# Optimization experiments

Measured on AMD Instinct MI355X. Metric: run time of the kernel, lower is better.

The kernel has to match this reference:

```python
import jax, jax.numpy as jnp
import numpy as np

DIM = 512
RANK = 64


def setup_inputs() -> dict:
    key = jax.random.key(0)
    ks = jax.random.split(key, 8)
    B, T, S = 2, 1024, 1024
    target_val = jax.random.normal(ks[0], (B, T, DIM), dtype=jnp.float32)
    source_val = jax.random.normal(ks[1], (B, S, DIM), dtype=jnp.float32)
    # Linear weights stored torch-style [out, in]
    Wt = jax.random.normal(ks[2], (RANK, DIM), dtype=jnp.float32) / np.sqrt(DIM)
    Ws = jax.random.normal(ks[3], (RANK, DIM), dtype=jnp.float32) / np.sqrt(DIM)
    wt_out = jax.random.normal(ks[4], (RANK,), dtype=jnp.float32) / np.sqrt(RANK)
    ws_out = jax.random.normal(ks[5], (RANK,), dtype=jnp.float32) / np.sqrt(RANK)
    interaction_weight = 0.02 * jax.random.normal(ks[6], (RANK,), dtype=jnp.float32)
    bias = jnp.zeros((), dtype=jnp.float32)
    return {
        'target_val': target_val,
        'source_val': source_val,
        'Wt': Wt,
        'Ws': Ws,
        'wt_out': wt_out,
        'ws_out': ws_out,
        'interaction_weight': interaction_weight,
        'bias': bias,
    }


def reference(target_val, source_val, Wt, Ws, wt_out, ws_out, interaction_weight, bias):
    # Project to low-rank width r
    pt = jnp.einsum('btd,rd->btr', target_val, Wt)   # [B,T,R]
    ps = jnp.einsum('bsd,rd->bsr', source_val, Ws)   # [B,S,R]
    target_linear = jnp.einsum('btr,r->bt', pt, wt_out)  # [B,T]
    source_linear = jnp.einsum('bsr,r->bs', ps, ws_out)  # [B,S]
    # Pairwise multiplicative interaction -> SiLU -> rank reduction
    interaction = jax.nn.silu(pt[:, :, None, :] * ps[:, None, :, :])  # [B,T,S,R]
    scores = jnp.einsum('btsr,r->bts', interaction, interaction_weight)
    scores = scores + target_linear[:, :, None] + source_linear[:, None, :] + bias
    return scores
```

## Files before the change

### kernel.cpp

```cpp
#include <hip/hip_runtime.h>

#define DIM   512
#define RANK  64
#define TDIM  1024
#define BB    2
#define NROWS (BB * TDIM)

__device__ __forceinline__ float fast_exp2(float x) { return __builtin_amdgcn_exp2f(x); }
__device__ __forceinline__ float fast_rcp(float x)  { return __builtin_amdgcn_rcpf(x); }

__global__ __launch_bounds__(256)
void proj_kernel(const float* __restrict__ tv, const float* __restrict__ sv,
                 const float* __restrict__ Wt, const float* __restrict__ Ws,
                 float* __restrict__ pt, float* __restrict__ ps)
{
    const int which = blockIdx.z;
    const float* X = which ? sv : tv;
    const float* W = which ? Ws : Wt;
    float* P       = which ? ps : pt;

    const int row0 = blockIdx.x * 64;
    const int kc   = blockIdx.y * 64;
    const int tid  = threadIdx.x;
    const int tx   = tid & 15;
    const int ty   = tid >> 4;

    __shared__ float xs[64][68];
    __shared__ float wsm[64][68];

#pragma unroll
    for (int p = 0; p < 4; p++) {
        const int r = (tid >> 4) + p * 16;
        const int c = (tid & 15) * 4;
        *(float4*)&xs[r][c]  = *(const float4*)&X[(size_t)(row0 + r) * DIM + kc + c];
        *(float4*)&wsm[r][c] = *(const float4*)&W[(size_t)r * DIM + kc + c];
    }
    __syncthreads();

    float acc[4][4];
#pragma unroll
    for (int i = 0; i < 4; i++)
#pragma unroll
        for (int j = 0; j < 4; j++) acc[i][j] = 0.f;

#pragma unroll 2
    for (int k4 = 0; k4 < 64; k4 += 4) {
        float4 a[4], b[4];
#pragma unroll
        for (int i = 0; i < 4; i++) a[i] = *(const float4*)&xs[ty + 16 * i][k4];
#pragma unroll
        for (int j = 0; j < 4; j++) b[j] = *(const float4*)&wsm[tx + 16 * j][k4];
#pragma unroll
        for (int i = 0; i < 4; i++)
#pragma unroll
            for (int j = 0; j < 4; j++) {
                acc[i][j] = fmaf(a[i].x, b[j].x, acc[i][j]);
                acc[i][j] = fmaf(a[i].y, b[j].y, acc[i][j]);
                acc[i][j] = fmaf(a[i].z, b[j].z, acc[i][j]);
                acc[i][j] = fmaf(a[i].w, b[j].w, acc[i][j]);
            }
    }

#pragma unroll
    for (int i = 0; i < 4; i++)
#pragma unroll
        for (int j = 0; j < 4; j++)
            atomicAdd(&P[(size_t)(row0 + ty + 16 * i) * RANK + tx + 16 * j], acc[i][j]);
}

__global__ __launch_bounds__(256)
void pair_kernel(const float* __restrict__ pt, const float* __restrict__ ps,
                 const float* __restrict__ wt_out, const float* __restrict__ ws_out,
                 const float* __restrict__ iw, const float* __restrict__ bias_p,
                 float* __restrict__ out)
{
    const int b  = blockIdx.z;
    const int t0 = blockIdx.y * 64;
    const int s0 = blockIdx.x * 64;
    const int tid = threadIdx.x;
    const int tx  = tid & 15;
    const int ty  = tid >> 4;

    __shared__ float pts[64][68];
    __shared__ float sts[64][68];
    __shared__ __align__(16) float wsh[64];
    __shared__ float tlsh[64];
    __shared__ float slsh[64];

    const float* ptb = pt + ((size_t)b * TDIM + t0) * RANK;
    const float* psb = ps + ((size_t)b * TDIM + s0) * RANK;

#pragma unroll
    for (int p = 0; p < 4; p++) {
        const int r = (tid >> 4) + p * 16;
        const int c = (tid & 15) * 4;
        *(float4*)&pts[r][c] = *(const float4*)&ptb[(size_t)r * RANK + c];
        *(float4*)&sts[r][c] = *(const float4*)&psb[(size_t)r * RANK + c];
    }
    if (tid < 64) wsh[tid] = iw[tid];
    __syncthreads();

    if (tid < 64) {
        float v = 0.f;
#pragma unroll 8
        for (int r = 0; r < RANK; r++) v = fmaf(pts[tid][r], wt_out[r], v);
        tlsh[tid] = v;
    } else if (tid < 128) {
        const int s = tid - 64;
        float v = 0.f;
#pragma unroll 8
        for (int r = 0; r < RANK; r++) v = fmaf(sts[s][r], ws_out[r], v);
        slsh[s] = v;
    }
    __syncthreads();

    const float bias = bias_p[0];

    float acc[4][4];
#pragma unroll
    for (int i = 0; i < 4; i++)
#pragma unroll
        for (int j = 0; j < 4; j++) acc[i][j] = 0.f;

    const float NL2E = -1.44269504088896340736f;

#pragma unroll 2
    for (int r4 = 0; r4 < RANK; r4 += 4) {
        const float4 w4 = *(const float4*)&wsh[r4];
        const float wv[4] = {w4.x, w4.y, w4.z, w4.w};

        float a2[4][4], wa[4][4], bv[4][4];
#pragma unroll
        for (int i = 0; i < 4; i++) {
            const float4 a = *(const float4*)&pts[ty + 16 * i][r4];
            const float av[4] = {a.x, a.y, a.z, a.w};
#pragma unroll
            for (int k = 0; k < 4; k++) {
                a2[i][k] = av[k] * NL2E;
                wa[i][k] = av[k] * wv[k];
            }
        }
#pragma unroll
        for (int j = 0; j < 4; j++) {
            const float4 v = *(const float4*)&sts[tx + 16 * j][r4];
            bv[j][0] = v.x; bv[j][1] = v.y; bv[j][2] = v.z; bv[j][3] = v.w;
        }

#pragma unroll
        for (int i = 0; i < 4; i++)
#pragma unroll
            for (int j = 0; j < 4; j++)
#pragma unroll
                for (int k = 0; k < 4; k++) {
                    const float t  = a2[i][k] * bv[j][k];
                    const float e  = fast_exp2(t);
                    const float rc = fast_rcp(1.0f + e);
                    acc[i][j] = fmaf(wa[i][k] * bv[j][k], rc, acc[i][j]);
                }
    }

#pragma unroll
    for (int i = 0; i < 4; i++) {
        const int t = t0 + ty + 16 * i;
        const float tl = tlsh[ty + 16 * i];
        float* orow = out + ((size_t)b * TDIM + t) * TDIM + s0;
#pragma unroll
        for (int j = 0; j < 4; j++) {
            orow[tx + 16 * j] = acc[i][j] + tl + slsh[tx + 16 * j] + bias;
        }
    }
}

extern "C" void kernel_launch(void* const* d_in, const int* in_sizes, int n_in,
                              void* d_out, int out_size, void* d_ws, size_t ws_size,
                              hipStream_t stream)
{
    const float* tv     = (const float*)d_in[0];
    const float* sv     = (const float*)d_in[1];
    const float* Wt     = (const float*)d_in[2];
    const float* Ws     = (const float*)d_in[3];
    const float* wt_out = (const float*)d_in[4];
    const float* ws_out = (const float*)d_in[5];
    const float* iw     = (const float*)d_in[6];
    const float* bias   = (const float*)d_in[7];
    float* out = (float*)d_out;

    float* pt = (float*)d_ws;
    float* ps = pt + (size_t)NROWS * RANK;

    hipMemsetAsync(d_ws, 0, 2 * (size_t)NROWS * RANK * sizeof(float), stream);

    dim3 pgrid(NROWS / 64, DIM / 64, 2);
    proj_kernel<<<pgrid, 256, 0, stream>>>(tv, sv, Wt, Ws, pt, ps);

    dim3 ggrid(TDIM / 64, TDIM / 64, BB);
    pair_kernel<<<ggrid, 256, 0, stream>>>(pt, ps, wt_out, ws_out, iw, bias, out);
}
```

Measured before the change: 117.9 us.

## Remove split-K atomics in projection and use packed float2 math in pair kernel

```diff
diff --git a/kernel.cpp b/kernel.cpp
--- a/kernel.cpp
+++ b/kernel.cpp
@@ -5,6 +5,9 @@
 #define TDIM  1024
 #define BB    2
 #define NROWS (BB * TDIM)
+
+typedef float v2f __attribute__((ext_vector_type(2)));
+typedef float v4f __attribute__((ext_vector_type(4)));
 
 __device__ __forceinline__ float fast_exp2(float x) { return __builtin_amdgcn_exp2f(x); }
 __device__ __forceinline__ float fast_rcp(float x)  { return __builtin_amdgcn_rcpf(x); }
@@ -14,58 +17,53 @@
                  const float* __restrict__ Wt, const float* __restrict__ Ws,
                  float* __restrict__ pt, float* __restrict__ ps)
 {
-    const int which = blockIdx.z;
+    const int which = blockIdx.y;
     const float* X = which ? sv : tv;
     const float* W = which ? Ws : Wt;
     float* P       = which ? ps : pt;
 
-    const int row0 = blockIdx.x * 64;
-    const int kc   = blockIdx.y * 64;
+    const int row0 = blockIdx.x * 16;
     const int tid  = threadIdx.x;
     const int tx   = tid & 15;
     const int ty   = tid >> 4;
 
-    __shared__ float xs[64][68];
+    __shared__ float xs[16][68];
     __shared__ float wsm[64][68];
 
+    v4f acc[4];
 #pragma unroll
-    for (int p = 0; p < 4; p++) {
-        const int r = (tid >> 4) + p * 16;
-        const int c = (tid & 15) * 4;
-        *(float4*)&xs[r][c]  = *(const float4*)&X[(size_t)(row0 + r) * DIM + kc + c];
-        *(float4*)&wsm[r][c] = *(const float4*)&W[(size_t)r * DIM + kc + c];
-    }
-    __syncthreads();
+    for (int j = 0; j < 4; j++) acc[j] = (v4f)0.f;
 
-    float acc[4][4];
+    for (int kc = 0; kc < DIM; kc += 64) {
+        {
+            const int r = tid >> 4;
+            const int c = (tid & 15) * 4;
+            *(v4f*)&xs[r][c] = *(const v4f*)&X[(size_t)(row0 + r) * DIM + kc + c];
 #pragma unroll
-    for (int i = 0; i < 4; i++)
-#pragma unroll
-        for (int j = 0; j < 4; j++) acc[i][j] = 0.f;
+            for (int p = 0; p < 4; p++) {
+                const int wr = (tid >> 4) + p * 16;
+                *(v4f*)&wsm[wr][c] = *(const v4f*)&W[(size_t)wr * DIM + kc + c];
+            }
+        }
+        __syncthreads();
 
-#pragma unroll 2
-    for (int k4 = 0; k4 < 64; k4 += 4) {
-        float4 a[4], b[4];
-#pragma unroll
-        for (int i = 0; i < 4; i++) a[i] = *(const float4*)&xs[ty + 16 * i][k4];
-#pragma unroll
-        for (int j = 0; j < 4; j++) b[j] = *(const float4*)&wsm[tx + 16 * j][k4];
-#pragma unroll
-        for (int i = 0; i < 4; i++)
+#pragma unroll 4
+        for (int k4 = 0; k4 < 64; k4 += 4) {
+            const v4f av = *(const v4f*)&xs[ty][k4];
 #pragma unroll
             for (int j = 0; j < 4; j++) {
-                acc[i][j] = fmaf(a[i].x, b[j].x, acc[i][j]);
-                acc[i][j] = fmaf(a[i].y, b[j].y, acc[i][j]);
-                acc[i][j] = fmaf(a[i].z, b[j].z, acc[i][j]);
-                acc[i][j] = fmaf(a[i].w, b[j].w, acc[i][j]);
+                const v4f bv = *(const v4f*)&wsm[tx + 16 * j][k4];
+                acc[j] += av * bv;
             }
+        }
+        __syncthreads();
     }
 
 #pragma unroll
-    for (int i = 0; i < 4; i++)
-#pragma unroll
-        for (int j = 0; j < 4; j++)
-            atomicAdd(&P[(size_t)(row0 + ty + 16 * i) * RANK + tx + 16 * j], acc[i][j]);
+    for (int j = 0; j < 4; j++) {
+        const float s = (acc[j].x + acc[j].y) + (acc[j].z + acc[j].w);
+        P[(size_t)(row0 + ty) * RANK + tx + 16 * j] = s;
+    }
 }
 
 __global__ __launch_bounds__(256)
@@ -94,8 +92,8 @@
     for (int p = 0; p < 4; p++) {
         const int r = (tid >> 4) + p * 16;
         const int c = (tid & 15) * 4;
-        *(float4*)&pts[r][c] = *(const float4*)&ptb[(size_t)r * RANK + c];
-        *(float4*)&sts[r][c] = *(const float4*)&psb[(size_t)r * RANK + c];
+        *(v4f*)&pts[r][c] = *(const v4f*)&ptb[(size_t)r * RANK + c];
+        *(v4f*)&sts[r][c] = *(const v4f*)&psb[(size_t)r * RANK + c];
     }
     if (tid < 64) wsh[tid] = iw[tid];
     __syncthreads();
@@ -115,48 +113,47 @@
     __syncthreads();
 
     const float bias = bias_p[0];
+    const float NL2E = -1.44269504088896340736f;
 
-    float acc[4][4];
+    v2f acc[4][4];
 #pragma unroll
     for (int i = 0; i < 4; i++)
 #pragma unroll
-        for (int j = 0; j < 4; j++) acc[i][j] = 0.f;
+        for (int j = 0; j < 4; j++) acc[i][j] = (v2f)0.f;
 
-    const float NL2E = -1.44269504088896340736f;
+    for (int r4 = 0; r4 < RANK; r4 += 4) {
+        const v4f wv = *(const v4f*)&wsh[r4];
 
-#pragma unroll 2
-    for (int r4 = 0; r4 < RANK; r4 += 4) {
-        const float4 w4 = *(const float4*)&wsh[r4];
-        const float wv[4] = {w4.x, w4.y, w4.z, w4.w};
-
-        float a2[4][4], wa[4][4], bv[4][4];
+        v4f a2[4], wa[4], bv[4];
 #pragma unroll
         for (int i = 0; i < 4; i++) {
-            const float4 a = *(const float4*)&pts[ty + 16 * i][r4];
-            const float av[4] = {a.x, a.y, a.z, a.w};
-#pragma unroll
-            for (int k = 0; k < 4; k++) {
-                a2[i][k] = av[k] * NL2E;
-                wa[i][k] = av[k] * wv[k];
-            }
+            const v4f av = *(const v4f*)&pts[ty + 16 * i][r4];
+            a2[i] = av * NL2E;
+            wa[i] = av * wv;
         }
 #pragma unroll
-        for (int j = 0; j < 4; j++) {
-            const float4 v = *(const float4*)&sts[tx + 16 * j][r4];
-            bv[j][0] = v.x; bv[j][1] = v.y; bv[j][2] = v.z; bv[j][3] = v.w;
-        }
+        for (int j = 0; j < 4; j++)
+            bv[j] = *(const v4f*)&sts[tx + 16 * j][r4];
 
 #pragma unroll
         for (int i = 0; i < 4; i++)
 #pragma unroll
-            for (int j = 0; j < 4; j++)
-#pragma unroll
-                for (int k = 0; k < 4; k++) {
-                    const float t  = a2[i][k] * bv[j][k];
-                    const float e  = fast_exp2(t);
-                    const float rc = fast_rcp(1.0f + e);
-                    acc[i][j] = fmaf(wa[i][k] * bv[j][k], rc, acc[i][j]);
-                }
+            for (int j = 0; j < 4; j++) {
+                const v2f t0v = a2[i].lo * bv[j].lo;
+                const v2f t1v = a2[i].hi * bv[j].hi;
+                v2f e0, e1;
+                e0.x = fast_exp2(t0v.x); e0.y = fast_exp2(t0v.y);
+                e1.x = fast_exp2(t1v.x); e1.y = fast_exp2(t1v.y);
+                const v2f d0 = e0 + 1.0f;
+                const v2f d1 = e1 + 1.0f;
+                v2f r0, r1;
+                r0.x = fast_rcp(d0.x); r0.y = fast_rcp(d0.y);
+                r1.x = fast_rcp(d1.x); r1.y = fast_rcp(d1.y);
+                const v2f w0 = wa[i].lo * bv[j].lo;
+                const v2f w1 = wa[i].hi * bv[j].hi;
+                acc[i][j] += w0 * r0;
+                acc[i][j] += w1 * r1;
+            }
     }
 
 #pragma unroll
@@ -166,7 +163,8 @@
         float* orow = out + ((size_t)b * TDIM + t) * TDIM + s0;
 #pragma unroll
         for (int j = 0; j < 4; j++) {
-            orow[tx + 16 * j] = acc[i][j] + tl + slsh[tx + 16 * j] + bias;
+            const float v = acc[i][j].x + acc[i][j].y;
+            orow[tx + 16 * j] = v + tl + slsh[tx + 16 * j] + bias;
         }
     }
 }
@@ -188,9 +186,7 @@
     float* pt = (float*)d_ws;
     float* ps = pt + (size_t)NROWS * RANK;
 
-    hipMemsetAsync(d_ws, 0, 2 * (size_t)NROWS * RANK * sizeof(float), stream);
-
-    dim3 pgrid(NROWS / 64, DIM / 64, 2);
+    dim3 pgrid(NROWS / 16, 2);
     proj_kernel<<<pgrid, 256, 0, stream>>>(tv, sv, Wt, Ws, pt, ps);
 
     dim3 ggrid(TDIM / 64, TDIM / 64, BB);
```

Result: no change. 118.6 us (+0.6%).

## Share one reciprocal across two sigmoids and halve pair-kernel tile height

Applied to the files above, without the earlier changes.

```diff
diff --git a/kernel.cpp b/kernel.cpp
--- a/kernel.cpp
+++ b/kernel.cpp
@@ -5,6 +5,8 @@
 #define TDIM  1024
 #define BB    2
 #define NROWS (BB * TDIM)
+
+typedef float v4f __attribute__((ext_vector_type(4)));
 
 __device__ __forceinline__ float fast_exp2(float x) { return __builtin_amdgcn_exp2f(x); }
 __device__ __forceinline__ float fast_rcp(float x)  { return __builtin_amdgcn_rcpf(x); }
@@ -32,8 +34,8 @@
     for (int p = 0; p < 4; p++) {
         const int r = (tid >> 4) + p * 16;
         const int c = (tid & 15) * 4;
-        *(float4*)&xs[r][c]  = *(const float4*)&X[(size_t)(row0 + r) * DIM + kc + c];
-        *(float4*)&wsm[r][c] = *(const float4*)&W[(size_t)r * DIM + kc + c];
+        *(v4f*)&xs[r][c]  = *(const v4f*)&X[(size_t)(row0 + r) * DIM + kc + c];
+        *(v4f*)&wsm[r][c] = *(const v4f*)&W[(size_t)r * DIM + kc + c];
     }
     __syncthreads();
 
@@ -45,11 +47,11 @@
 
 #pragma unroll 2
     for (int k4 = 0; k4 < 64; k4 += 4) {
-        float4 a[4], b[4];
-#pragma unroll
-        for (int i = 0; i < 4; i++) a[i] = *(const float4*)&xs[ty + 16 * i][k4];
-#pragma unroll
-        for (int j = 0; j < 4; j++) b[j] = *(const float4*)&wsm[tx + 16 * j][k4];
+        v4f a[4], b[4];
+#pragma unroll
+        for (int i = 0; i < 4; i++) a[i] = *(const v4f*)&xs[ty + 16 * i][k4];
+#pragma unroll
+        for (int j = 0; j < 4; j++) b[j] = *(const v4f*)&wsm[tx + 16 * j][k4];
 #pragma unroll
         for (int i = 0; i < 4; i++)
 #pragma unroll
@@ -75,37 +77,42 @@
                  float* __restrict__ out)
 {
     const int b  = blockIdx.z;
-    const int t0 = blockIdx.y * 64;
+    const int t0 = blockIdx.y * 32;
     const int s0 = blockIdx.x * 64;
     const int tid = threadIdx.x;
     const int tx  = tid & 15;
     const int ty  = tid >> 4;
 
-    __shared__ float pts[64][68];
+    __shared__ float pts[32][68];
     __shared__ float sts[64][68];
     __shared__ __align__(16) float wsh[64];
-    __shared__ float tlsh[64];
+    __shared__ float tlsh[32];
     __shared__ float slsh[64];
 
     const float* ptb = pt + ((size_t)b * TDIM + t0) * RANK;
     const float* psb = ps + ((size_t)b * TDIM + s0) * RANK;
 
+#pragma unroll
+    for (int p = 0; p < 2; p++) {
+        const int r = (tid >> 4) + p * 16;
+        const int c = (tid & 15) * 4;
+        *(v4f*)&pts[r][c] = *(const v4f*)&ptb[(size_t)r * RANK + c];
+    }
 #pragma unroll
     for (int p = 0; p < 4; p++) {
         const int r = (tid >> 4) + p * 16;
         const int c = (tid & 15) * 4;
-        *(float4*)&pts[r][c] = *(const float4*)&ptb[(size_t)r * RANK + c];
-        *(float4*)&sts[r][c] = *(const float4*)&psb[(size_t)r * RANK + c];
+        *(v4f*)&sts[r][c] = *(const v4f*)&psb[(size_t)r * RANK + c];
     }
     if (tid < 64) wsh[tid] = iw[tid];
     __syncthreads();
 
-    if (tid < 64) {
+    if (tid < 32) {
         float v = 0.f;
 #pragma unroll 8
         for (int r = 0; r < RANK; r++) v = fmaf(pts[tid][r], wt_out[r], v);
         tlsh[tid] = v;
-    } else if (tid < 128) {
+    } else if (tid >= 64 && tid < 128) {
         const int s = tid - 64;
         float v = 0.f;
 #pragma unroll 8
@@ -115,52 +122,59 @@
     __syncthreads();
 
     const float bias = bias_p[0];
-
-    float acc[4][4];
-#pragma unroll
-    for (int i = 0; i < 4; i++)
+    const float NL2E = -1.44269504088896340736f;
+
+    float acc[2][4];
+#pragma unroll
+    for (int i = 0; i < 2; i++)
 #pragma unroll
         for (int j = 0; j < 4; j++) acc[i][j] = 0.f;
 
-    const float NL2E = -1.44269504088896340736f;
-
-#pragma unroll 2
     for (int r4 = 0; r4 < RANK; r4 += 4) {
-        const float4 w4 = *(const float4*)&wsh[r4];
-        const float wv[4] = {w4.x, w4.y, w4.z, w4.w};
-
-        float a2[4][4], wa[4][4], bv[4][4];
-#pragma unroll
-        for (int i = 0; i < 4; i++) {
-            const float4 a = *(const float4*)&pts[ty + 16 * i][r4];
-            const float av[4] = {a.x, a.y, a.z, a.w};
+        const v4f wv4 = *(const v4f*)&wsh[r4];
+        const float wv[4] = {wv4.x, wv4.y, wv4.z, wv4.w};
+
+        float a2[2][4], wa[2][4], bv[4][4];
+#pragma unroll
+        for (int i = 0; i < 2; i++) {
+            const v4f av = *(const v4f*)&pts[ty + 16 * i][r4];
+            const float avv[4] = {av.x, av.y, av.z, av.w};
 #pragma unroll
             for (int k = 0; k < 4; k++) {
-                a2[i][k] = av[k] * NL2E;
-                wa[i][k] = av[k] * wv[k];
+                a2[i][k] = avv[k] * NL2E;
+                wa[i][k] = avv[k] * wv[k];
             }
         }
 #pragma unroll
         for (int j = 0; j < 4; j++) {
-            const float4 v = *(const float4*)&sts[tx + 16 * j][r4];
-            bv[j][0] = v.x; bv[j][1] = v.y; bv[j][2] = v.z; bv[j][3] = v.w;
+            const v4f bb = *(const v4f*)&sts[tx + 16 * j][r4];
+            bv[j][0] = bb.x; bv[j][1] = bb.y; bv[j][2] = bb.z; bv[j][3] = bb.w;
         }
 
 #pragma unroll
-        for (int i = 0; i < 4; i++)
+        for (int i = 0; i < 2; i++)
 #pragma unroll
             for (int j = 0; j < 4; j++)
 #pragma unroll
-                for (int k = 0; k < 4; k++) {
-                    const float t  = a2[i][k] * bv[j][k];
-                    const float e  = fast_exp2(t);
-                    const float rc = fast_rcp(1.0f + e);
-                    acc[i][j] = fmaf(wa[i][k] * bv[j][k], rc, acc[i][j]);
+                for (int k2 = 0; k2 < 4; k2 += 2) {
+                    const float t0v = a2[i][k2]     * bv[j][k2];
+                    const float t1v = a2[i][k2 + 1] * bv[j][k2 + 1];
+                    const float e0  = fast_exp2(t0v);
+                    const float e1  = fast_exp2(t1v);
+                    const float d0  = e0 + 1.0f;
+                    const float d1  = e1 + 1.0f;
+                    const float r   = fast_rcp(d0 * d1);
+                    const float s0  = r * d1;
+                    const float s1  = r * d0;
+                    const float wz0 = wa[i][k2]     * bv[j][k2];
+                    const float wz1 = wa[i][k2 + 1] * bv[j][k2 + 1];
+                    acc[i][j] = fmaf(wz0, s0, acc[i][j]);
+                    acc[i][j] = fmaf(wz1, s1, acc[i][j]);
                 }
     }
 
 #pragma unroll
-    for (int i = 0; i < 4; i++) {
+    for (int i = 0; i < 2; i++) {
         const int t = t0 + ty + 16 * i;
         const float tl = tlsh[ty + 16 * i];
         float* orow = out + ((size_t)b * TDIM + t) * TDIM + s0;
@@ -193,6 +207,6 @@
     dim3 pgrid(NROWS / 64, DIM / 64, 2);
     proj_kernel<<<pgrid, 256, 0, stream>>>(tv, sv, Wt, Ws, pt, ps);
 
-    dim3 ggrid(TDIM / 64, TDIM / 64, BB);
+    dim3 ggrid(TDIM / 64, TDIM / 32, BB);
     pair_kernel<<<ggrid, 256, 0, stream>>>(pt, ps, wt_out, ws_out, iw, bias, out);
 }
```

Result: faster. 114.7 us (-2.7%).
